# Performance work log

Hardware: AMD Instinct MI355X
Metric: run time of the kernel (lower is better)

The kernel has to match this reference:

```python
import jax, jax.numpy as jnp
import numpy as np

N_ATOMS = 10000
N_EDGES = 320000
F = 128
LN_EPS = 1e-5
VN_EPS = 1e-8


def _layer_norm(x, gamma, beta):
    mu = jnp.mean(x, axis=-1, keepdims=True)
    var = jnp.mean(jnp.square(x - mu), axis=-1, keepdims=True)
    return (x - mu) * jax.lax.rsqrt(var + LN_EPS) * gamma + beta


def _vector_norm(x):
    # Equivariant RMS normalization: per-channel vector norms, RMS over channels.
    sq = jnp.sum(jnp.square(x), axis=1, keepdims=True)          # [N,1,F]
    rms = jnp.sqrt(jnp.mean(sq, axis=-1, keepdims=True) + VN_EPS)  # [N,1,1]
    return x / rms


def setup_inputs() -> dict:
    key = jax.random.key(0)
    ks = jax.random.split(key, 16)
    rn = lambda k, shape, s=1.0: jax.random.normal(k, shape, dtype=jnp.float32) * s
    w_s = 0.05  # small init scale for weights
    return {
        "h": rn(ks[0], (N_ATOMS, 1, F)),
        "v": rn(ks[1], (N_ATOMS, 3, F)),
        "H": rn(ks[2], (N_ATOMS, 1, F)),
        "V": rn(ks[3], (N_ATOMS, 3, F)),
        "Wij": rn(ks[4], (N_EDGES, 1, 3 * F)),
        "dir_ij": rn(ks[5], (N_EDGES, 3)),
        "W1": rn(ks[6], (F, F), w_s),
        "b1": jnp.zeros((F,), jnp.float32),
        "W2": rn(ks[7], (F, 3 * F), w_s),
        "b2": jnp.zeros((3 * F,), jnp.float32),
        "Wmix": rn(ks[8], (F, 2 * F), w_s),
        "Wh_remain": rn(ks[9], (F, F), w_s),
        "Wh_forget": rn(ks[10], (F, F), w_s),
        "Wv_remain": rn(ks[11], (F, 1), w_s),
        "gamma": jnp.ones((F,), jnp.float32),
        "beta": jnp.zeros((F,), jnp.float32),
        "idx_i": jnp.sort(jax.random.randint(ks[12], (N_EDGES,), 0, N_ATOMS)),
        "idx_j": jax.random.randint(ks[13], (N_EDGES,), 0, N_ATOMS),
        "n_atoms": N_ATOMS,
    }


def reference(h, v, H, V, Wij, dir_ij, W1, b1, W2, b2, Wmix,
              Wh_remain, Wh_forget, Wv_remain, gamma, beta,
              idx_i, idx_j, n_atoms):
    # interatomic context net: Dense(F,F,silu) -> Dense(F,3F)
    X = jax.nn.silu(H @ W1 + b1) @ W2 + b2            # [N,1,3F]
    Hj = X[idx_j]                                      # [E,1,3F]
    Vj = V[idx_j]                                      # [E,3,F]
    Xe = Wij * Hj                                      # [E,1,3F]
    dh_e, dvR, dvv = jnp.split(Xe, 3, axis=-1)         # each [E,1,F]
    dh = jax.ops.segment_sum(dh_e, idx_i, num_segments=n_atoms)  # [N,1,F]
    dv_e = dvR * dir_ij[:, :, None] + dvv * Vj         # [E,3,F]
    dv = jax.ops.segment_sum(dv_e, idx_i, num_segments=n_atoms)  # [N,3,F]

    v_mix = v @ Wmix                                   # [N,3,2F]
    v_V, v_W = jnp.split(v_mix, 2, axis=-1)
    ctx = jnp.sum(v_V * v_W, axis=1, keepdims=True)    # [N,1,F]

    q = _layer_norm(h + dh @ Wh_remain + (dh @ Wh_forget) * ctx, gamma, beta)
    mu = _vector_norm(v + dv + (dh @ Wv_remain) * v)
    return q, mu
```

## Files before the change

kernel.cpp:

```cpp
#include <hip/hip_runtime.h>
#include <math.h>

#define FDIM 128
#define F3   384

static constexpr int K1_R = 16;
static constexpr int K2_R = 16;
static constexpr int K4_R = 8;
static constexpr int CHUNK = 64;

__global__ __launch_bounds__(128) void k1_ctxnet(
    const float* __restrict__ H,  const float* __restrict__ W1,
    const float* __restrict__ b1, const float* __restrict__ W2,
    const float* __restrict__ b2, float* __restrict__ X, int N)
{
    __shared__ float sH[K1_R][FDIM];
    __shared__ float sT[K1_R][FDIM];
    const int f  = threadIdx.x;
    const int n0 = blockIdx.x * K1_R;

    for (int r = 0; r < K1_R; ++r) {
        int n = n0 + r;
        sH[r][f] = (n < N) ? H[(size_t)n * FDIM + f] : 0.f;
    }
    __syncthreads();

    float acc[K1_R];
    #pragma unroll
    for (int r = 0; r < K1_R; ++r) acc[r] = 0.f;
    #pragma unroll 8
    for (int a = 0; a < FDIM; ++a) {
        float w = W1[a * FDIM + f];
        #pragma unroll
        for (int r = 0; r < K1_R; ++r) acc[r] = fmaf(sH[r][a], w, acc[r]);
    }
    float bb = b1[f];
    #pragma unroll
    for (int r = 0; r < K1_R; ++r) {
        float t = acc[r] + bb;
        sT[r][f] = t / (1.f + expf(-t));
    }
    __syncthreads();

    float a0[K1_R], a1[K1_R], a2[K1_R];
    #pragma unroll
    for (int r = 0; r < K1_R; ++r) { a0[r] = 0.f; a1[r] = 0.f; a2[r] = 0.f; }
    #pragma unroll 8
    for (int a = 0; a < FDIM; ++a) {
        float w0 = W2[a * F3 + f];
        float w1 = W2[a * F3 + FDIM + f];
        float w2 = W2[a * F3 + 2 * FDIM + f];
        #pragma unroll
        for (int r = 0; r < K1_R; ++r) {
            float t = sT[r][a];
            a0[r] = fmaf(t, w0, a0[r]);
            a1[r] = fmaf(t, w1, a1[r]);
            a2[r] = fmaf(t, w2, a2[r]);
        }
    }
    float c0 = b2[f], c1 = b2[FDIM + f], c2 = b2[2 * FDIM + f];
    for (int r = 0; r < K1_R; ++r) {
        int n = n0 + r;
        if (n < N) {
            X[(size_t)n * F3 + f]            = a0[r] + c0;
            X[(size_t)n * F3 + FDIM + f]     = a1[r] + c1;
            X[(size_t)n * F3 + 2 * FDIM + f] = a2[r] + c2;
        }
    }
}

__global__ __launch_bounds__(128) void k2_ctx(
    const float* __restrict__ v, const float* __restrict__ Wmix,
    float* __restrict__ ctx, int N)
{
    __shared__ float sv[3][K2_R][FDIM];
    const int f  = threadIdx.x;
    const int n0 = blockIdx.x * K2_R;

    for (int r = 0; r < K2_R; ++r) {
        int n = n0 + r;
        for (int d = 0; d < 3; ++d)
            sv[d][r][f] = (n < N) ? v[((size_t)n * 3 + d) * FDIM + f] : 0.f;
    }
    __syncthreads();

    float cacc[K2_R];
    #pragma unroll
    for (int r = 0; r < K2_R; ++r) cacc[r] = 0.f;

    for (int d = 0; d < 3; ++d) {
        float aV[K2_R], aW[K2_R];
        #pragma unroll
        for (int r = 0; r < K2_R; ++r) { aV[r] = 0.f; aW[r] = 0.f; }
        #pragma unroll 8
        for (int a = 0; a < FDIM; ++a) {
            float w0 = Wmix[a * (2 * FDIM) + f];
            float w1 = Wmix[a * (2 * FDIM) + FDIM + f];
            #pragma unroll
            for (int r = 0; r < K2_R; ++r) {
                float t = sv[d][r][a];
                aV[r] = fmaf(t, w0, aV[r]);
                aW[r] = fmaf(t, w1, aW[r]);
            }
        }
        #pragma unroll
        for (int r = 0; r < K2_R; ++r) cacc[r] = fmaf(aV[r], aW[r], cacc[r]);
    }
    for (int r = 0; r < K2_R; ++r) {
        int n = n0 + r;
        if (n < N) ctx[(size_t)n * FDIM + f] = cacc[r];
    }
}

__device__ inline int lower_bound_i(const int* __restrict__ a, int n, int val) {
    int lo = 0, hi = n;
    while (lo < hi) {
        int m = (lo + hi) >> 1;
        if (a[m] < val) lo = m + 1; else hi = m;
    }
    return lo;
}

__global__ __launch_bounds__(256) void k3_edges(
    const float* __restrict__ X, const float* __restrict__ V,
    const float* __restrict__ Wij, const float* __restrict__ dir_ij,
    const int* __restrict__ idx_i, const int* __restrict__ idx_j,
    float* __restrict__ dh, float* __restrict__ dv, int E)
{
    const int n    = blockIdx.x;
    const int tid  = threadIdx.x;
    const int f    = tid & 127;
    const int half = tid >> 7;

    __shared__ int   sj[CHUNK];
    __shared__ float sd[CHUNK][4];
    __shared__ float sacc[4][FDIM];

    const int e0 = lower_bound_i(idx_i, E, n);
    const int e1 = lower_bound_i(idx_i, E, n + 1);

    float adh = 0.f, a0 = 0.f, a1 = 0.f, a2 = 0.f;

    for (int base = e0; base < e1; base += CHUNK) {
        const int cnt = (e1 - base < CHUNK) ? (e1 - base) : CHUNK;
        if (tid < cnt) sj[tid] = idx_j[base + tid];
        for (int t = tid; t < 3 * cnt; t += 256)
            sd[t / 3][t % 3] = dir_ij[(size_t)base * 3 + t];
        __syncthreads();

        int k = half;
        for (; k + 2 < cnt; k += 4) {
            const int eA = base + k, eB = base + k + 2;
            const int jA = sj[k],    jB = sj[k + 2];
            const float* wA = Wij + (size_t)eA * F3;
            const float* wB = Wij + (size_t)eB * F3;
            const float* xA = X + (size_t)jA * F3;
            const float* xB = X + (size_t)jB * F3;
            const float* vA = V + (size_t)jA * F3;
            const float* vB = V + (size_t)jB * F3;
            float wA0 = wA[f], wA1 = wA[FDIM + f], wA2 = wA[2 * FDIM + f];
            float xA0 = xA[f], xA1 = xA[FDIM + f], xA2 = xA[2 * FDIM + f];
            float vA0 = vA[f], vA1 = vA[FDIM + f], vA2 = vA[2 * FDIM + f];
            float wB0 = wB[f], wB1 = wB[FDIM + f], wB2 = wB[2 * FDIM + f];
            float xB0 = xB[f], xB1 = xB[FDIM + f], xB2 = xB[2 * FDIM + f];
            float vB0 = vB[f], vB1 = vB[FDIM + f], vB2 = vB[2 * FDIM + f];
            float dA0 = sd[k][0],     dA1 = sd[k][1],     dA2 = sd[k][2];
            float dB0 = sd[k + 2][0], dB1 = sd[k + 2][1], dB2 = sd[k + 2][2];

            adh = fmaf(wA0, xA0, adh);
            float rA = wA1 * xA1, sA = wA2 * xA2;
            a0 = fmaf(rA, dA0, fmaf(sA, vA0, a0));
            a1 = fmaf(rA, dA1, fmaf(sA, vA1, a1));
            a2 = fmaf(rA, dA2, fmaf(sA, vA2, a2));

            adh = fmaf(wB0, xB0, adh);
            float rB = wB1 * xB1, sB = wB2 * xB2;
            a0 = fmaf(rB, dB0, fmaf(sB, vB0, a0));
            a1 = fmaf(rB, dB1, fmaf(sB, vB1, a1));
            a2 = fmaf(rB, dB2, fmaf(sB, vB2, a2));
        }
        for (; k < cnt; k += 2) {
            const int e = base + k;
            const int j = sj[k];
            const float* w = Wij + (size_t)e * F3;
            const float* x = X + (size_t)j * F3;
            const float* vv = V + (size_t)j * F3;
            float w0 = w[f], w1 = w[FDIM + f], w2 = w[2 * FDIM + f];
            float x0 = x[f], x1 = x[FDIM + f], x2 = x[2 * FDIM + f];
            float v0 = vv[f], v1 = vv[FDIM + f], v2 = vv[2 * FDIM + f];
            float d0 = sd[k][0], d1 = sd[k][1], d2 = sd[k][2];
            adh = fmaf(w0, x0, adh);
            float r = w1 * x1, s = w2 * x2;
            a0 = fmaf(r, d0, fmaf(s, v0, a0));
            a1 = fmaf(r, d1, fmaf(s, v1, a1));
            a2 = fmaf(r, d2, fmaf(s, v2, a2));
        }
        __syncthreads();
    }

    if (half == 1) {
        sacc[0][f] = adh; sacc[1][f] = a0; sacc[2][f] = a1; sacc[3][f] = a2;
    }
    __syncthreads();
    if (half == 0) {
        adh += sacc[0][f]; a0 += sacc[1][f]; a1 += sacc[2][f]; a2 += sacc[3][f];
        dh[(size_t)n * FDIM + f]          = adh;
        dv[(size_t)n * F3 + f]            = a0;
        dv[(size_t)n * F3 + FDIM + f]     = a1;
        dv[(size_t)n * F3 + 2 * FDIM + f] = a2;
    }
}

__device__ inline float block_reduce_sum_128(float val, float* tmp) {
    #pragma unroll
    for (int o = 32; o > 0; o >>= 1) val += __shfl_down(val, o, 64);
    const int tid = threadIdx.x;
    if ((tid & 63) == 0) tmp[tid >> 6] = val;
    __syncthreads();
    float r = tmp[0] + tmp[1];
    __syncthreads();
    return r;
}

__global__ __launch_bounds__(128) void k4_epilogue(
    const float* __restrict__ h,   const float* __restrict__ v,
    const float* __restrict__ dh,  const float* __restrict__ dv,
    const float* __restrict__ ctx,
    const float* __restrict__ Whr, const float* __restrict__ Whf,
    const float* __restrict__ Wvr,
    const float* __restrict__ gamma, const float* __restrict__ beta,
    float* __restrict__ q, float* __restrict__ mu, int N)
{
    __shared__ float sdh[K4_R][FDIM];
    __shared__ float sred[2];
    const int f  = threadIdx.x;
    const int n0 = blockIdx.x * K4_R;

    for (int r = 0; r < K4_R; ++r) {
        int n = n0 + r;
        sdh[r][f] = (n < N) ? dh[(size_t)n * FDIM + f] : 0.f;
    }
    __syncthreads();

    float accR[K4_R], accF[K4_R];
    #pragma unroll
    for (int r = 0; r < K4_R; ++r) { accR[r] = 0.f; accF[r] = 0.f; }
    #pragma unroll 8
    for (int a = 0; a < FDIM; ++a) {
        float wr = Whr[a * FDIM + f];
        float wf = Whf[a * FDIM + f];
        #pragma unroll
        for (int r = 0; r < K4_R; ++r) {
            accR[r] = fmaf(sdh[r][a], wr, accR[r]);
            accF[r] = fmaf(sdh[r][a], wf, accF[r]);
        }
    }

    const float wv = Wvr[f];
    const float g  = gamma[f];
    const float bt = beta[f];

    for (int r = 0; r < K4_R; ++r) {
        int n = n0 + r;
        if (n >= N) break;

        float s = block_reduce_sum_128(sdh[r][f] * wv, sred);

        float u    = h[(size_t)n * FDIM + f] + accR[r] + accF[r] * ctx[(size_t)n * FDIM + f];
        float mean = block_reduce_sum_128(u, sred) * (1.f / 128.f);
        float dlt  = u - mean;
        float var  = block_reduce_sum_128(dlt * dlt, sred) * (1.f / 128.f);
        q[(size_t)n * FDIM + f] = dlt * rsqrtf(var + 1e-5f) * g + bt;

        float sc = 1.f + s;
        float x0 = fmaf(v[((size_t)n * 3 + 0) * FDIM + f], sc, dv[(size_t)n * F3 + f]);
        float x1 = fmaf(v[((size_t)n * 3 + 1) * FDIM + f], sc, dv[(size_t)n * F3 + FDIM + f]);
        float x2 = fmaf(v[((size_t)n * 3 + 2) * FDIM + f], sc, dv[(size_t)n * F3 + 2 * FDIM + f]);
        float sq  = x0 * x0 + x1 * x1 + x2 * x2;
        float tot = block_reduce_sum_128(sq, sred) * (1.f / 128.f);
        float inv = rsqrtf(tot + 1e-8f);
        mu[((size_t)n * 3 + 0) * FDIM + f] = x0 * inv;
        mu[((size_t)n * 3 + 1) * FDIM + f] = x1 * inv;
        mu[((size_t)n * 3 + 2) * FDIM + f] = x2 * inv;
    }
}

extern "C" void kernel_launch(void* const* d_in, const int* in_sizes, int n_in,
                              void* d_out, int out_size, void* d_ws, size_t ws_size,
                              hipStream_t stream)
{
    const float* h     = (const float*)d_in[0];
    const float* v     = (const float*)d_in[1];
    const float* H     = (const float*)d_in[2];
    const float* V     = (const float*)d_in[3];
    const float* Wij   = (const float*)d_in[4];
    const float* dir   = (const float*)d_in[5];
    const float* W1    = (const float*)d_in[6];
    const float* b1    = (const float*)d_in[7];
    const float* W2    = (const float*)d_in[8];
    const float* b2    = (const float*)d_in[9];
    const float* Wmix  = (const float*)d_in[10];
    const float* Whr   = (const float*)d_in[11];
    const float* Whf   = (const float*)d_in[12];
    const float* Wvr   = (const float*)d_in[13];
    const float* gamma = (const float*)d_in[14];
    const float* beta  = (const float*)d_in[15];
    const int*   idx_i = (const int*)d_in[16];
    const int*   idx_j = (const int*)d_in[17];

    const int N = in_sizes[0] / FDIM;
    const int E = in_sizes[16];

    float* ws  = (float*)d_ws;
    float* X   = ws;
    float* ctx = X   + (size_t)N * F3;
    float* dh  = ctx + (size_t)N * FDIM;
    float* dv  = dh  + (size_t)N * FDIM;

    float* q   = (float*)d_out;
    float* mu  = q + (size_t)N * FDIM;

    hipLaunchKernelGGL(k1_ctxnet, dim3((N + K1_R - 1) / K1_R), dim3(128), 0, stream,
                       H, W1, b1, W2, b2, X, N);
    hipLaunchKernelGGL(k2_ctx, dim3((N + K2_R - 1) / K2_R), dim3(128), 0, stream,
                       v, Wmix, ctx, N);
    hipLaunchKernelGGL(k3_edges, dim3(N), dim3(256), 0, stream,
                       X, V, Wij, dir, idx_i, idx_j, dh, dv, E);
    hipLaunchKernelGGL(k4_epilogue, dim3((N + K4_R - 1) / K4_R), dim3(128), 0, stream,
                       h, v, dh, dv, ctx, Whr, Whf, Wvr, gamma, beta, q, mu, N);
}
```

Before: 1.046 ms.

## Precompute segment offsets, deepen edge-loop loads, add nontemporal Wij loads, shrink row tiles

Adds a small kernel that computes the CSR segment offsets once with binary search, so each edge block no longer runs two binary searches over idx_i. The edge loop now issues loads for four edges before doing the FMAs, raising memory-level parallelism, and streams the Wij rows with nontemporal loads to keep them from polluting cache. The dense kernels use halved row tiles and smaller unroll factors, giving more blocks and lower register pressure at the cost of less weight reuse. The extra kernel launch and the workspace area for seg add a little overhead.

```diff
diff --git a/kernel.cpp b/kernel.cpp
--- a/kernel.cpp
+++ b/kernel.cpp
@@ -4,10 +4,24 @@
 #define FDIM 128
 #define F3   384
 
-static constexpr int K1_R = 16;
-static constexpr int K2_R = 16;
-static constexpr int K4_R = 8;
+static constexpr int K1_R = 8;
+static constexpr int K2_R = 8;
+static constexpr int K4_R = 4;
 static constexpr int CHUNK = 64;
+
+__global__ __launch_bounds__(256) void k0_seg(
+    const int* __restrict__ idx_i, int* __restrict__ seg, int E, int N)
+{
+    int n = blockIdx.x * 256 + threadIdx.x;
+    if (n > N) return;
+    if (n == N) { seg[n] = E; return; }
+    int lo = 0, hi = E;
+    while (lo < hi) {
+        int m = (lo + hi) >> 1;
+        if (idx_i[m] < n) lo = m + 1; else hi = m;
+    }
+    seg[n] = lo;
+}
 
 __global__ __launch_bounds__(128) void k1_ctxnet(
     const float* __restrict__ H,  const float* __restrict__ W1,
@@ -28,7 +42,7 @@
     float acc[K1_R];
     #pragma unroll
     for (int r = 0; r < K1_R; ++r) acc[r] = 0.f;
-    #pragma unroll 8
+    #pragma unroll 4
     for (int a = 0; a < FDIM; ++a) {
         float w = W1[a * FDIM + f];
         #pragma unroll
@@ -45,7 +59,7 @@
     float a0[K1_R], a1[K1_R], a2[K1_R];
     #pragma unroll
     for (int r = 0; r < K1_R; ++r) { a0[r] = 0.f; a1[r] = 0.f; a2[r] = 0.f; }
-    #pragma unroll 8
+    #pragma unroll 4
     for (int a = 0; a < FDIM; ++a) {
         float w0 = W2[a * F3 + f];
         float w1 = W2[a * F3 + FDIM + f];
@@ -92,7 +106,7 @@
         float aV[K2_R], aW[K2_R];
         #pragma unroll
         for (int r = 0; r < K2_R; ++r) { aV[r] = 0.f; aW[r] = 0.f; }
-        #pragma unroll 8
+        #pragma unroll 4
         for (int a = 0; a < FDIM; ++a) {
             float w0 = Wmix[a * (2 * FDIM) + f];
             float w1 = Wmix[a * (2 * FDIM) + FDIM + f];
@@ -112,20 +126,11 @@
     }
 }
 
-__device__ inline int lower_bound_i(const int* __restrict__ a, int n, int val) {
-    int lo = 0, hi = n;
-    while (lo < hi) {
-        int m = (lo + hi) >> 1;
-        if (a[m] < val) lo = m + 1; else hi = m;
-    }
-    return lo;
-}
-
 __global__ __launch_bounds__(256) void k3_edges(
     const float* __restrict__ X, const float* __restrict__ V,
     const float* __restrict__ Wij, const float* __restrict__ dir_ij,
-    const int* __restrict__ idx_i, const int* __restrict__ idx_j,
-    float* __restrict__ dh, float* __restrict__ dv, int E)
+    const int* __restrict__ seg, const int* __restrict__ idx_j,
+    float* __restrict__ dh, float* __restrict__ dv)
 {
     const int n    = blockIdx.x;
     const int tid  = threadIdx.x;
@@ -136,10 +141,29 @@
     __shared__ float sd[CHUNK][4];
     __shared__ float sacc[4][FDIM];
 
-    const int e0 = lower_bound_i(idx_i, E, n);
-    const int e1 = lower_bound_i(idx_i, E, n + 1);
+    const int e0 = seg[n];
+    const int e1 = seg[n + 1];
 
     float adh = 0.f, a0 = 0.f, a1 = 0.f, a2 = 0.f;
+
+#define EDGE_LOAD(kk, W0,W1_,W2_,X0,X1,X2,V0,V1,V2,D0,D1,D2)                   \
+    {   const int e_ = base + (kk); const int j_ = sj[(kk)];                   \
+        const float* w_ = Wij + (size_t)e_ * F3;                               \
+        const float* x_ = X   + (size_t)j_ * F3;                               \
+        const float* q_ = V   + (size_t)j_ * F3;                               \
+        W0 = __builtin_nontemporal_load(w_ + f);                               \
+        W1_ = __builtin_nontemporal_load(w_ + FDIM + f);                       \
+        W2_ = __builtin_nontemporal_load(w_ + 2 * FDIM + f);                   \
+        X0 = x_[f]; X1 = x_[FDIM + f]; X2 = x_[2 * FDIM + f];                  \
+        V0 = q_[f]; V1 = q_[FDIM + f]; V2 = q_[2 * FDIM + f];                  \
+        D0 = sd[(kk)][0]; D1 = sd[(kk)][1]; D2 = sd[(kk)][2]; }
+
+#define EDGE_FMA(W0,W1_,W2_,X0,X1,X2,V0,V1,V2,D0,D1,D2)                       \
+    {   adh = fmaf(W0, X0, adh);                                               \
+        float r_ = W1_ * X1, s_ = W2_ * X2;                                    \
+        a0 = fmaf(r_, D0, fmaf(s_, V0, a0));                                   \
+        a1 = fmaf(r_, D1, fmaf(s_, V1, a1));                                   \
+        a2 = fmaf(r_, D2, fmaf(s_, V2, a2)); }
 
     for (int base = e0; base < e1; base += CHUNK) {
         const int cnt = (e1 - base < CHUNK) ? (e1 - base) : CHUNK;
@@ -149,54 +173,29 @@
         __syncthreads();
 
         int k = half;
-        for (; k + 2 < cnt; k += 4) {
-            const int eA = base + k, eB = base + k + 2;
-            const int jA = sj[k],    jB = sj[k + 2];
-            const float* wA = Wij + (size_t)eA * F3;
-            const float* wB = Wij + (size_t)eB * F3;
-            const float* xA = X + (size_t)jA * F3;
-            const float* xB = X + (size_t)jB * F3;
-            const float* vA = V + (size_t)jA * F3;
-            const float* vB = V + (size_t)jB * F3;
-            float wA0 = wA[f], wA1 = wA[FDIM + f], wA2 = wA[2 * FDIM + f];
-            float xA0 = xA[f], xA1 = xA[FDIM + f], xA2 = xA[2 * FDIM + f];
-            float vA0 = vA[f], vA1 = vA[FDIM + f], vA2 = vA[2 * FDIM + f];
-            float wB0 = wB[f], wB1 = wB[FDIM + f], wB2 = wB[2 * FDIM + f];
-            float xB0 = xB[f], xB1 = xB[FDIM + f], xB2 = xB[2 * FDIM + f];
-            float vB0 = vB[f], vB1 = vB[FDIM + f], vB2 = vB[2 * FDIM + f];
-            float dA0 = sd[k][0],     dA1 = sd[k][1],     dA2 = sd[k][2];
-            float dB0 = sd[k + 2][0], dB1 = sd[k + 2][1], dB2 = sd[k + 2][2];
-
-            adh = fmaf(wA0, xA0, adh);
-            float rA = wA1 * xA1, sA = wA2 * xA2;
-            a0 = fmaf(rA, dA0, fmaf(sA, vA0, a0));
-            a1 = fmaf(rA, dA1, fmaf(sA, vA1, a1));
-            a2 = fmaf(rA, dA2, fmaf(sA, vA2, a2));
-
-            adh = fmaf(wB0, xB0, adh);
-            float rB = wB1 * xB1, sB = wB2 * xB2;
-            a0 = fmaf(rB, dB0, fmaf(sB, vB0, a0));
-            a1 = fmaf(rB, dB1, fmaf(sB, vB1, a1));
-            a2 = fmaf(rB, dB2, fmaf(sB, vB2, a2));
+        for (; k + 6 < cnt; k += 8) {
+            float wA0,wA1,wA2,xA0,xA1,xA2,vA0,vA1,vA2,dA0,dA1,dA2;
+            float wB0,wB1,wB2,xB0,xB1,xB2,vB0,vB1,vB2,dB0,dB1,dB2;
+            float wC0,wC1,wC2,xC0,xC1,xC2,vC0,vC1,vC2,dC0,dC1,dC2;
+            float wD0,wD1,wD2,xD0,xD1,xD2,vD0,vD1,vD2,dD0,dD1,dD2;
+            EDGE_LOAD(k,     wA0,wA1,wA2,xA0,xA1,xA2,vA0,vA1,vA2,dA0,dA1,dA2)
+            EDGE_LOAD(k + 2, wB0,wB1,wB2,xB0,xB1,xB2,vB0,vB1,vB2,dB0,dB1,dB2)
+            EDGE_LOAD(k + 4, wC0,wC1,wC2,xC0,xC1,xC2,vC0,vC1,vC2,dC0,dC1,dC2)
+            EDGE_LOAD(k + 6, wD0,wD1,wD2,xD0,xD1,xD2,vD0,vD1,vD2,dD0,dD1,dD2)
+            EDGE_FMA(wA0,wA1,wA2,xA0,xA1,xA2,vA0,vA1,vA2,dA0,dA1,dA2)
+            EDGE_FMA(wB0,wB1,wB2,xB0,xB1,xB2,vB0,vB1,vB2,dB0,dB1,dB2)
+            EDGE_FMA(wC0,wC1,wC2,xC0,xC1,xC2,vC0,vC1,vC2,dC0,dC1,dC2)
+            EDGE_FMA(wD0,wD1,wD2,xD0,xD1,xD2,vD0,vD1,vD2,dD0,dD1,dD2)
         }
         for (; k < cnt; k += 2) {
-            const int e = base + k;
-            const int j = sj[k];
-            const float* w = Wij + (size_t)e * F3;
-            const float* x = X + (size_t)j * F3;
-            const float* vv = V + (size_t)j * F3;
-            float w0 = w[f], w1 = w[FDIM + f], w2 = w[2 * FDIM + f];
-            float x0 = x[f], x1 = x[FDIM + f], x2 = x[2 * FDIM + f];
-            float v0 = vv[f], v1 = vv[FDIM + f], v2 = vv[2 * FDIM + f];
-            float d0 = sd[k][0], d1 = sd[k][1], d2 = sd[k][2];
-            adh = fmaf(w0, x0, adh);
-            float r = w1 * x1, s = w2 * x2;
-            a0 = fmaf(r, d0, fmaf(s, v0, a0));
-            a1 = fmaf(r, d1, fmaf(s, v1, a1));
-            a2 = fmaf(r, d2, fmaf(s, v2, a2));
+            float w0,w1,w2,x0,x1,x2,v0,v1,v2,d0,d1,d2;
+            EDGE_LOAD(k, w0,w1,w2,x0,x1,x2,v0,v1,v2,d0,d1,d2)
+            EDGE_FMA(w0,w1,w2,x0,x1,x2,v0,v1,v2,d0,d1,d2)
         }
         __syncthreads();
     }
+#undef EDGE_LOAD
+#undef EDGE_FMA
 
     if (half == 1) {
         sacc[0][f] = adh; sacc[1][f] = a0; sacc[2][f] = a1; sacc[3][f] = a2;
@@ -245,7 +244,7 @@
     float accR[K4_R], accF[K4_R];
     #pragma unroll
     for (int r = 0; r < K4_R; ++r) { accR[r] = 0.f; accF[r] = 0.f; }
-    #pragma unroll 8
+    #pragma unroll 4
     for (int a = 0; a < FDIM; ++a) {
         float wr = Whr[a * FDIM + f];
         float wf = Whf[a * FDIM + f];
@@ -316,16 +315,19 @@
     float* ctx = X   + (size_t)N * F3;
     float* dh  = ctx + (size_t)N * FDIM;
     float* dv  = dh  + (size_t)N * FDIM;
+    int*   seg = (int*)(dv + (size_t)N * F3);
 
     float* q   = (float*)d_out;
     float* mu  = q + (size_t)N * FDIM;
 
+    hipLaunchKernelGGL(k0_seg, dim3((N + 256) / 256), dim3(256), 0, stream,
+                       idx_i, seg, E, N);
     hipLaunchKernelGGL(k1_ctxnet, dim3((N + K1_R - 1) / K1_R), dim3(128), 0, stream,
                        H, W1, b1, W2, b2, X, N);
     hipLaunchKernelGGL(k2_ctx, dim3((N + K2_R - 1) / K2_R), dim3(128), 0, stream,
                        v, Wmix, ctx, N);
     hipLaunchKernelGGL(k3_edges, dim3(N), dim3(256), 0, stream,
-                       X, V, Wij, dir, idx_i, idx_j, dh, dv, E);
+                       X, V, Wij, dir, seg, idx_j, dh, dv);
     hipLaunchKernelGGL(k4_epilogue, dim3((N + K4_R - 1) / K4_R), dim3(128), 0, stream,
                        h, v, dh, dv, ctx, Whr, Whf, Wvr, gamma, beta, q, mu, N);
 }
```

Result: faster. 887.8 us (-15.1%).
